# Kernel tuning notes

Hardware: AMD Instinct MI355X
Metric: run time of the kernel (lower is better)

Reference implementation:

```python
import jax, jax.numpy as jnp
import numpy as np

S, B, D, H, E, K, FF = 1024, 8, 768, 12, 8, 2, 3072


def _ln(x, w, b, eps=1e-5):
    m = x.mean(-1, keepdims=True)
    v = ((x - m) ** 2).mean(-1, keepdims=True)
    return (x - m) / jnp.sqrt(v + eps) * w + b


def setup_inputs() -> dict:
    key = jax.random.key(0)
    ks = jax.random.split(key, 12)
    s = 0.02
    return {
        "x": jax.random.normal(ks[0], (S, B, D), dtype=jnp.float32),
        "ln1_w": jnp.ones((D,), jnp.float32),
        "ln1_b": jnp.zeros((D,), jnp.float32),
        "in_proj_w": jax.random.normal(ks[1], (3 * D, D), jnp.float32) * s,
        "in_proj_b": jnp.zeros((3 * D,), jnp.float32),
        "out_proj_w": jax.random.normal(ks[2], (D, D), jnp.float32) * s,
        "out_proj_b": jnp.zeros((D,), jnp.float32),
        "ln2_w": jnp.ones((D,), jnp.float32),
        "ln2_b": jnp.zeros((D,), jnp.float32),
        "gate_w": jax.random.normal(ks[3], (E, D), jnp.float32) * s,
        "w1": jax.random.normal(ks[4], (E, D, FF), jnp.float32) * s,
        "b1": jnp.zeros((E, FF), jnp.float32),
        "w2": jax.random.normal(ks[5], (E, FF, D), jnp.float32) * s,
        "b2": jnp.zeros((E, D), jnp.float32),
    }


def reference(x, ln1_w, ln1_b, in_proj_w, in_proj_b, out_proj_w, out_proj_b,
              ln2_w, ln2_b, gate_w, w1, b1, w2, b2):
    s, b, d = x.shape
    hd = d // H
    # --- self attention (nn.MultiheadAttention, seq-first, no mask) ---
    h = _ln(x, ln1_w, ln1_b)
    qkv = h @ in_proj_w.T + in_proj_b            # [S, B, 3D]
    q, k, v = jnp.split(qkv, 3, axis=-1)

    def heads(t):
        return t.reshape(s, b, H, hd).transpose(1, 2, 0, 3)  # [B, H, S, hd]

    q, k, v = heads(q) * (hd ** -0.5), heads(k), heads(v)
    att = jax.nn.softmax(jnp.einsum('bhqd,bhkd->bhqk', q, k), axis=-1)
    o = jnp.einsum('bhqk,bhkd->bhqd', att, v).transpose(2, 0, 1, 3).reshape(s, b, d)
    o = o @ out_proj_w.T + out_proj_b
    x = x + o
    # --- MoE FFN ---
    h2 = _ln(x, ln2_w, ln2_b)
    tok = h2.reshape(-1, d)                      # [T, D], T = S*B
    logits = tok @ gate_w.T                      # [T, E]
    rw = jax.nn.softmax(logits.astype(jnp.float32), axis=-1)
    rw_top, sel = jax.lax.top_k(rw, K)           # [T, K]
    rw_top = rw_top / rw_top.sum(-1, keepdims=True)
    rw_top = rw_top.astype(tok.dtype)
    out = jnp.zeros_like(tok)
    for e in range(E):  # small fixed expert loop; math matches gather/scatter dispatch
        we = jnp.where(sel == e, rw_top, 0.0).sum(-1)       # [T] combine weight
        mid = tok @ w1[e] + b1[e]
        mid = mid * jax.nn.sigmoid(1.702 * mid)              # QuickGELU
        out = out + we[:, None] * (mid @ w2[e] + b2[e])
    return x + out.reshape(s, b, d), logits
```

## Files before the change

### kernel.cpp

```cpp
#include <hip/hip_runtime.h>
#include <stdint.h>

#define S_LEN  1024
#define BATCH  8
#define DMODEL 768
#define NHEAD  12
#define HDIM   64
#define NEXP   8
#define FFDIM  3072
#define NTOK   8192
#define D3     2304
#define NGATH  16384
#define MAXWL  136

typedef unsigned short u16;
typedef unsigned int   u32;
typedef __attribute__((ext_vector_type(8))) short bf16x8;
typedef __attribute__((ext_vector_type(4))) float f32x4;
typedef __attribute__((ext_vector_type(4))) short s16x4;

__device__ __forceinline__ u16 f2bf(float f){
  u32 x = __float_as_uint(f);
  x += 0x7fffu + ((x >> 16) & 1u);
  return (u16)(x >> 16);
}
__device__ __forceinline__ float bf2f(u16 u){
  return __uint_as_float(((u32)u) << 16);
}
__device__ __forceinline__ u32 pkbf(float a, float b){
  u32 d; asm("v_cvt_pk_bf16_f32 %0, %1, %2" : "=v"(d) : "v"(a), "v"(b)); return d;
}
__device__ __forceinline__ void gl_lds16(const void* g, void* l){
  __builtin_amdgcn_global_load_lds(
      (const __attribute__((address_space(1))) u32*)(uintptr_t)g,
      (__attribute__((address_space(3))) u32*)(u32)(uintptr_t)l,
      16, 0, 0);
}
__device__ __forceinline__ int swz64(int r){ return ((r & 7) ^ ((r >> 3) & 7)) << 4; }

__global__ __launch_bounds__(256)
void cvt_bf16(const float* __restrict__ in, u16* __restrict__ out, int n)
{
  int i = (blockIdx.x * 256 + threadIdx.x) * 4;
  if (i + 3 < n) {
    float4 v = *(const float4*)(in + i);
    out[i]     = f2bf(v.x);
    out[i + 1] = f2bf(v.y);
    out[i + 2] = f2bf(v.z);
    out[i + 3] = f2bf(v.w);
  }
}

__global__ __launch_bounds__(256)
void transpose_cvt(const float* __restrict__ in, u16* __restrict__ out, int rows, int cols)
{
  __shared__ float tile[32][33];
  const size_t eo = (size_t)blockIdx.z * rows * cols;
  in  += eo; out += eo;
  const int bx = blockIdx.x * 32, by = blockIdx.y * 32;
  const int tx = threadIdx.x, ty = threadIdx.y;
  #pragma unroll
  for (int i = 0; i < 4; i++)
    tile[ty + i * 8][tx] = in[(size_t)(by + ty + i * 8) * cols + bx + tx];
  __syncthreads();
  #pragma unroll
  for (int i = 0; i < 4; i++)
    out[(size_t)(bx + ty + i * 8) * rows + by + tx] = f2bf(tile[tx][ty + i * 8]);
}

__global__ __launch_bounds__(256)
void ln_fwd(const float* __restrict__ x, const float* __restrict__ w, const float* __restrict__ b,
            u16* __restrict__ out)
{
  const int t = blockIdx.x, tid = threadIdx.x;
  const float* xr = x + (size_t)t * DMODEL;
  const float v0 = xr[tid], v1 = xr[tid + 256], v2 = xr[tid + 512];
  float s = v0 + v1 + v2, ss = v0 * v0 + v1 * v1 + v2 * v2;
  #pragma unroll
  for (int d = 1; d < 64; d <<= 1) { s += __shfl_xor(s, d); ss += __shfl_xor(ss, d); }
  __shared__ float rs[4], rq[4];
  if ((tid & 63) == 0) { rs[tid >> 6] = s; rq[tid >> 6] = ss; }
  __syncthreads();
  s  = rs[0] + rs[1] + rs[2] + rs[3];
  ss = rq[0] + rq[1] + rq[2] + rq[3];
  const float mean = s * (1.f / DMODEL);
  const float rstd = rsqrtf(ss * (1.f / DMODEL) - mean * mean + 1e-5f);
  u16* orow = out + (size_t)t * DMODEL;
  orow[tid]       = f2bf((v0 - mean) * rstd * w[tid]       + b[tid]);
  orow[tid + 256] = f2bf((v1 - mean) * rstd * w[tid + 256] + b[tid + 256]);
  orow[tid + 512] = f2bf((v2 - mean) * rstd * w[tid + 512] + b[tid + 512]);
}

__global__ __launch_bounds__(256)
void ln2_gate(const float* __restrict__ x1, const float* __restrict__ w, const float* __restrict__ b,
              const float* __restrict__ gate_w, u16* __restrict__ h2,
              float* __restrict__ logits, float* __restrict__ selw, int* __restrict__ seli)
{
  const int t = blockIdx.x, tid = threadIdx.x;
  const float* xr = x1 + (size_t)t * DMODEL;
  const float v0 = xr[tid], v1 = xr[tid + 256], v2 = xr[tid + 512];
  float s = v0 + v1 + v2, ss = v0 * v0 + v1 * v1 + v2 * v2;
  #pragma unroll
  for (int d = 1; d < 64; d <<= 1) { s += __shfl_xor(s, d); ss += __shfl_xor(ss, d); }
  __shared__ float rs[4], rq[4];
  if ((tid & 63) == 0) { rs[tid >> 6] = s; rq[tid >> 6] = ss; }
  __syncthreads();
  s  = rs[0] + rs[1] + rs[2] + rs[3];
  ss = rq[0] + rq[1] + rq[2] + rq[3];
  const float mean = s * (1.f / DMODEL);
  const float rstd = rsqrtf(ss * (1.f / DMODEL) - mean * mean + 1e-5f);
  __shared__ float row[DMODEL];
  const float y0 = (v0 - mean) * rstd * w[tid]       + b[tid];
  const float y1 = (v1 - mean) * rstd * w[tid + 256] + b[tid + 256];
  const float y2 = (v2 - mean) * rstd * w[tid + 512] + b[tid + 512];
  row[tid] = y0; row[tid + 256] = y1; row[tid + 512] = y2;
  u16* hr = h2 + (size_t)t * DMODEL;
  hr[tid] = f2bf(y0); hr[tid + 256] = f2bf(y1); hr[tid + 512] = f2bf(y2);
  __syncthreads();
  __shared__ float lg[NEXP];
  if (tid < 64) {
    const int e = tid >> 3, j = tid & 7;
    const float* gw = gate_w + e * DMODEL;
    float a = 0.f;
    for (int d = j; d < DMODEL; d += 8) a += row[d] * gw[d];
    a += __shfl_xor(a, 1); a += __shfl_xor(a, 2); a += __shfl_xor(a, 4);
    if (j == 0) lg[e] = a;
  }
  __syncthreads();
  if (tid < NEXP) logits[(size_t)t * NEXP + tid] = lg[tid];
  if (tid == 0) {
    int ia = 0, ib = -1;
    float va = -1e30f, vb = -1e30f;
    #pragma unroll
    for (int e = 0; e < NEXP; e++) {
      const float p = lg[e];
      if (p > va)      { vb = va; ib = ia; va = p; ia = e; }
      else if (p > vb) { vb = p; ib = e; }
    }
    const float pb = __expf(vb - va);
    const float inv = 1.f / (1.f + pb);
    selw[2 * t]     = inv;
    selw[2 * t + 1] = pb * inv;
    seli[2 * t]     = ia;
    seli[2 * t + 1] = ib;
  }
}

__global__ __launch_bounds__(256)
void route_count(const int* __restrict__ seli, int* __restrict__ blkcnt)
{
  __shared__ int c[NEXP];
  const int tid = threadIdx.x;
  if (tid < NEXP) c[tid] = 0;
  __syncthreads();
  const int t = blockIdx.x * 256 + tid;
  atomicAdd(&c[seli[2 * t]], 1);
  atomicAdd(&c[seli[2 * t + 1]], 1);
  __syncthreads();
  if (tid < NEXP) blkcnt[blockIdx.x * NEXP + tid] = c[tid];
}

__global__ void route_scan(const int* __restrict__ blkcnt, int* __restrict__ offs,
                           int* __restrict__ blkbase, int* __restrict__ wl, int* __restrict__ nwork)
{
  const int tid = threadIdx.x;
  __shared__ int tot[NEXP];
  __shared__ int off_s[NEXP + 1];
  if (tid < NEXP) {
    int s = 0;
    for (int blk = 0; blk < 32; blk++) s += blkcnt[blk * NEXP + tid];
    tot[tid] = s;
  }
  __syncthreads();
  if (tid == 0) {
    int run = 0;
    for (int e = 0; e < NEXP; e++) { off_s[e] = run; run += tot[e]; }
    off_s[NEXP] = run;
    int nw = 0;
    for (int e = 0; e < NEXP; e++) {
      const int nb = (tot[e] + 127) >> 7;
      for (int i2 = 0; i2 < nb; i2++) wl[nw++] = (e << 16) | i2;
    }
    nwork[0] = nw;
  }
  __syncthreads();
  if (tid <= NEXP) offs[tid] = off_s[tid];
  if (tid < NEXP) {
    int run = off_s[tid];
    for (int blk = 0; blk < 32; blk++) { blkbase[blk * NEXP + tid] = run; run += blkcnt[blk * NEXP + tid]; }
  }
}

__global__ __launch_bounds__(256)
void route_place(const int* __restrict__ seli, const int* __restrict__ blkbase,
                 int* __restrict__ perm, int* __restrict__ posmap)
{
  __shared__ int cnts[2][4][NEXP];
  __shared__ int base[NEXP];
  const int tid = threadIdx.x, l = tid & 63, w = tid >> 6, blk = blockIdx.x;
  const int t = blk * 256 + tid;
  const unsigned long long ltm = (1ull << l) - 1ull;
  int my_e[2], my_r[2];
  my_e[0] = seli[2 * t]; my_e[1] = seli[2 * t + 1];
  my_r[0] = 0; my_r[1] = 0;
  if (tid < NEXP) base[tid] = blkbase[blk * NEXP + tid];
  #pragma unroll
  for (int k = 0; k < 2; k++) {
    #pragma unroll
    for (int ee = 0; ee < NEXP; ee++) {
      const unsigned long long msk = __ballot(my_e[k] == ee);
      if (my_e[k] == ee) my_r[k] = (int)__popcll(msk & ltm);
      if (l == ee) cnts[k][w][ee] = (int)__popcll(msk);
    }
  }
  __syncthreads();
  #pragma unroll
  for (int k = 0; k < 2; k++) {
    const int e = my_e[k];
    int pre = base[e];
    for (int k2 = 0; k2 < 2; k2++)
      for (int w2 = 0; w2 < 4; w2++)
        if (k2 < k || (k2 == k && w2 < w)) pre += cnts[k2][w2][e];
    const int pos = pre + my_r[k];
    perm[pos] = t;
    posmap[2 * t + k] = pos;
  }
}

template<int MODE>
__global__ __launch_bounds__(256)
void gemm128(const u16* __restrict__ A, const u16* __restrict__ Bw,
             int M, int N, int Kd,
             const float* __restrict__ bias, const float* __restrict__ resid,
             void* __restrict__ outp,
             const int* __restrict__ perm, const int* __restrict__ offs,
             const int* __restrict__ wl, const int* __restrict__ nwork)
{
  __shared__ u16 As[128 * 64];
  __shared__ u16 Bs[128 * 64];
  const int tid = threadIdx.x;
  const int l   = tid & 63;
  const int w   = tid >> 6;
  const int wm  = w >> 1, wn = w & 1;
  const int bn  = blockIdx.y;

  int gbase = 0, cnt = M, e = 0, bm = blockIdx.x;
  if (MODE >= 2) {
    if (blockIdx.x >= nwork[0]) return;
    const int wk = wl[blockIdx.x];
    e  = wk >> 16;
    bm = wk & 0xffff;
    gbase = offs[e];
    cnt   = offs[e + 1] - gbase;
  }
  const u16*   Bp = Bw   + (MODE >= 2 ? (size_t)e * N * Kd : 0);
  const float* bp = bias + (MODE >= 2 ? e * N : 0);

  int arow[4], acol[4], brow[4];
  #pragma unroll
  for (int i = 0; i < 4; i++) {
    const int c = tid + 256 * i;
    const int r = c >> 3;
    const int f = (r & 7) ^ ((r >> 3) & 7);
    acol[i] = ((c & 7) ^ f) * 8;
    brow[i] = bn * 128 + r;
    int g;
    if (MODE == 2)      { int gp = gbase + bm * 128 + r; if (gp > NGATH - 1) gp = NGATH - 1; g = perm[gp]; }
    else if (MODE == 3) { int gp = gbase + bm * 128 + r; if (gp > NGATH - 1) gp = NGATH - 1; g = gp; }
    else                g = bm * 128 + r;
    arow[i] = g;
  }

  f32x4 acc[4][4] = {};
  const int nk = Kd >> 6;
  for (int kt = 0; kt < nk; kt++) {
    const int kb = kt * 64;
    #pragma unroll
    for (int i = 0; i < 4; i++) {
      gl_lds16(A  + (size_t)arow[i] * Kd + kb + acol[i], &As[(i * 256 + w * 64) * 8]);
      gl_lds16(Bp + (size_t)brow[i] * Kd + kb + acol[i], &Bs[(i * 256 + w * 64) * 8]);
    }
    __syncthreads();
    #pragma unroll
    for (int ks = 0; ks < 2; ks++) {
      bf16x8 af[4], bv[4];
      #pragma unroll
      for (int m = 0; m < 4; m++) {
        const int row = wm * 64 + m * 16 + (l & 15);
        af[m] = *(const bf16x8*)((const char*)As +
                  ((row * 128 + ks * 64 + (l >> 4) * 16) ^ swz64(row)));
      }
      #pragma unroll
      for (int n = 0; n < 4; n++) {
        const int row = wn * 64 + n * 16 + (l & 15);
        bv[n] = *(const bf16x8*)((const char*)Bs +
                  ((row * 128 + ks * 64 + (l >> 4) * 16) ^ swz64(row)));
      }
      #pragma unroll
      for (int m = 0; m < 4; m++)
        #pragma unroll
        for (int n = 0; n < 4; n++)
          acc[m][n] = __builtin_amdgcn_mfma_f32_16x16x32_bf16(bv[n], af[m], acc[m][n], 0, 0, 0);
    }
    __syncthreads();
  }

  f32x4 biasv[4];
  int   c0[4];
  #pragma unroll
  for (int n = 0; n < 4; n++) {
    c0[n] = bn * 128 + wn * 64 + n * 16 + ((l >> 4) << 2);
    biasv[n] = *(const f32x4*)(bp + c0[n]);
  }
  #pragma unroll
  for (int m = 0; m < 4; m++) {
    const int row = bm * 128 + wm * 64 + m * 16 + (l & 15);
    #pragma unroll
    for (int n = 0; n < 4; n++) {
      f32x4 v = acc[m][n] + biasv[n];
      if (MODE == 0) {
        *(uint2*)((u16*)outp + (size_t)row * N + c0[n]) =
            make_uint2(pkbf(v[0], v[1]), pkbf(v[2], v[3]));
      } else if (MODE == 1) {
        const size_t o = (size_t)row * N + c0[n];
        f32x4 rv = *(const f32x4*)(resid + o);
        v += rv;
        *(f32x4*)((float*)outp + o) = v;
      } else if (MODE == 2) {
        if (row < cnt) {
          #pragma unroll
          for (int r = 0; r < 4; r++)
            v[r] = v[r] * __builtin_amdgcn_rcpf(1.f + __expf(-1.702f * v[r]));
          *(uint2*)((u16*)outp + (size_t)(gbase + row) * FFDIM + c0[n]) =
              make_uint2(pkbf(v[0], v[1]), pkbf(v[2], v[3]));
        }
      } else {
        if (row < cnt)
          *(uint2*)((u16*)outp + (size_t)(gbase + row) * DMODEL + c0[n]) =
              make_uint2(pkbf(v[0], v[1]), pkbf(v[2], v[3]));
      }
    }
  }
}

__global__ __launch_bounds__(256)
void attn_fwd(const u16* __restrict__ qkv, u16* __restrict__ o)
{
  __shared__ u16 Ksw[64 * 64];
  __shared__ u16 Vt [64 * 64];
  __shared__ u16 Pl [4 * 16 * 64];
  const int tid = threadIdx.x;
  const int l   = tid & 63, w = tid >> 6;
  const int qt  = blockIdx.x;
  const int b_  = blockIdx.y / NHEAD;
  const int hh  = blockIdx.y % NHEAD;

  const int qrow = qt * 64 + w * 16 + (l & 15);
  const size_t qoff = ((size_t)(qrow * BATCH + b_)) * D3 + hh * HDIM + (l >> 4) * 8;
  const bf16x8 qa0 = *(const bf16x8*)&qkv[qoff];
  const bf16x8 qa1 = *(const bf16x8*)&qkv[qoff + 32];

  f32x4 oacc[4] = {};
  float m_[4], l_[4];
  #pragma unroll
  for (int r = 0; r < 4; r++) { m_[r] = -1e30f; l_[r] = 0.f; }

  u16* Pw = Pl + w * 1024;
  const int pswz = swz64(l & 15);

  for (int kt = 0; kt < 16; kt++) {
    #pragma unroll
    for (int i = 0; i < 2; i++) {
      const int c = tid + 256 * i;
      const int key = c >> 3, dimb = (c & 7) * 8;
      const size_t gb = ((size_t)((kt * 64 + key) * BATCH + b_)) * D3 + hh * HDIM + dimb;
      const bf16x8 kd = *(const bf16x8*)&qkv[gb + DMODEL];
      const bf16x8 vd = *(const bf16x8*)&qkv[gb + 2 * DMODEL];
      *(bf16x8*)((char*)Ksw + ((key * 128 + dimb * 2) ^ swz64(key))) = kd;
      #pragma unroll
      for (int j = 0; j < 8; j++) {
        const int dim = dimb + j;
        *(u16*)((char*)Vt + ((dim * 128 + key * 2) ^ swz64(dim))) = (u16)vd[j];
      }
    }
    __syncthreads();

    f32x4 sc[4] = {};
    #pragma unroll
    for (int kb2 = 0; kb2 < 4; kb2++) {
      const int key = kb2 * 16 + (l & 15);
      const int ksz = swz64(key);
      #pragma unroll
      for (int ks = 0; ks < 2; ks++) {
        const bf16x8 kf = *(const bf16x8*)((char*)Ksw +
            ((key * 128 + (ks * 32 + (l >> 4) * 8) * 2) ^ ksz));
        sc[kb2] = __builtin_amdgcn_mfma_f32_16x16x32_bf16(ks ? qa1 : qa0, kf, sc[kb2], 0, 0, 0);
      }
    }
    #pragma unroll
    for (int kb2 = 0; kb2 < 4; kb2++)
      #pragma unroll
      for (int r = 0; r < 4; r++) sc[kb2][r] *= 0.125f;

    float nm[4], corr[4], ps[4];
    #pragma unroll
    for (int r = 0; r < 4; r++) {
      float pm = fmaxf(fmaxf(sc[0][r], sc[1][r]), fmaxf(sc[2][r], sc[3][r]));
      pm = fmaxf(pm, __shfl_xor(pm, 1));
      pm = fmaxf(pm, __shfl_xor(pm, 2));
      pm = fmaxf(pm, __shfl_xor(pm, 4));
      pm = fmaxf(pm, __shfl_xor(pm, 8));
      nm[r]   = fmaxf(m_[r], pm);
      corr[r] = __expf(m_[r] - nm[r]);
      m_[r]   = nm[r];
      ps[r]   = 0.f;
    }
    #pragma unroll
    for (int kb2 = 0; kb2 < 4; kb2++) {
      #pragma unroll
      for (int r = 0; r < 4; r++) {
        const float p = __expf(sc[kb2][r] - nm[r]);
        ps[r] += p;
        const int prow = (l >> 4) * 4 + r;
        const int pcol = kb2 * 16 + (l & 15);
        *(u16*)((char*)Pw + ((prow * 128 + pcol * 2) ^ swz64(prow))) = f2bf(p);
      }
    }
    #pragma unroll
    for (int r = 0; r < 4; r++) {
      float s = ps[r];
      s += __shfl_xor(s, 1); s += __shfl_xor(s, 2);
      s += __shfl_xor(s, 4); s += __shfl_xor(s, 8);
      l_[r] = l_[r] * corr[r] + s;
      #pragma unroll
      for (int ob = 0; ob < 4; ob++) oacc[ob][r] *= corr[r];
    }

    #pragma unroll
    for (int ob = 0; ob < 4; ob++) {
      const int dim = ob * 16 + (l & 15);
      const int vsz = swz64(dim);
      #pragma unroll
      for (int ks = 0; ks < 2; ks++) {
        const int kko = (ks * 32 + (l >> 4) * 8) * 2;
        const bf16x8 pf = *(const bf16x8*)((char*)Pw + (((l & 15) * 128 + kko) ^ pswz));
        const bf16x8 vf = *(const bf16x8*)((char*)Vt + ((dim * 128 + kko) ^ vsz));
        oacc[ob] = __builtin_amdgcn_mfma_f32_16x16x32_bf16(pf, vf, oacc[ob], 0, 0, 0);
      }
    }
    __syncthreads();
  }

  #pragma unroll
  for (int r = 0; r < 4; r++) {
    const float inv = 1.f / l_[r];
    const int qs = qt * 64 + w * 16 + (l >> 4) * 4 + r;
    #pragma unroll
    for (int ob = 0; ob < 4; ob++)
      o[((size_t)(qs * BATCH + b_)) * DMODEL + hh * HDIM + ob * 16 + (l & 15)] =
          f2bf(oacc[ob][r] * inv);
  }
}

__global__ __launch_bounds__(192)
void moe_combine(const float* __restrict__ x1, const u16* __restrict__ eout,
                 const int* __restrict__ posmap, const float* __restrict__ selw,
                 float* __restrict__ out)
{
  const int t = blockIdx.x, j = threadIdx.x;
  const int p0 = posmap[2 * t], p1 = posmap[2 * t + 1];
  const float w0 = selw[2 * t], w1 = selw[2 * t + 1];
  const float4 xv = ((const float4*)(x1 + (size_t)t * DMODEL))[j];
  const s16x4 a = ((const s16x4*)(eout + (size_t)p0 * DMODEL))[j];
  const s16x4 c = ((const s16x4*)(eout + (size_t)p1 * DMODEL))[j];
  float4 r;
  r.x = xv.x + w0 * bf2f((u16)a[0]) + w1 * bf2f((u16)c[0]);
  r.y = xv.y + w0 * bf2f((u16)a[1]) + w1 * bf2f((u16)c[1]);
  r.z = xv.z + w0 * bf2f((u16)a[2]) + w1 * bf2f((u16)c[2]);
  r.w = xv.w + w0 * bf2f((u16)a[3]) + w1 * bf2f((u16)c[3]);
  ((float4*)(out + (size_t)t * DMODEL))[j] = r;
}

#define MB (1ull << 20)
static const size_t OFF_H    = 0;
static const size_t OFF_QKV  = 16 * MB;
static const size_t OFF_O    = 54 * MB;
static const size_t OFF_IPW  = 67 * MB;
static const size_t OFF_OPW  = 71 * MB;
static const size_t OFF_MID  = 0;
static const size_t OFF_X1   = 101 * MB;
static const size_t OFF_H2   = 127 * MB;
static const size_t OFF_W1T  = 140 * MB;
static const size_t OFF_W2T  = 178 * MB;
static const size_t OFF_EOUT = 216 * MB;
static const size_t OFF_SELW = 242 * MB;
static const size_t OFF_PERM = 242 * MB + (1 << 16);
static const size_t OFF_POS  = 242 * MB + (2 << 16);
static const size_t OFF_SELI = 242 * MB + (3 << 16);
static const size_t OFF_BCNT = 242 * MB + (4 << 16);
static const size_t OFF_BBASE= 242 * MB + (4 << 16) + 4096;
static const size_t OFF_OFFS = 242 * MB + (4 << 16) + 8192;
static const size_t OFF_WL   = 242 * MB + (5 << 16);
static const size_t OFF_NW   = 242 * MB + (5 << 16) + 1024;

extern "C" void kernel_launch(void* const* d_in, const int* in_sizes, int n_in,
                              void* d_out, int out_size, void* d_ws, size_t ws_size,
                              hipStream_t stream)
{
  const float* x     = (const float*)d_in[0];
  const float* ln1w  = (const float*)d_in[1];
  const float* ln1b  = (const float*)d_in[2];
  const float* ipw_f = (const float*)d_in[3];
  const float* ipb   = (const float*)d_in[4];
  const float* opw_f = (const float*)d_in[5];
  const float* opb   = (const float*)d_in[6];
  const float* ln2w  = (const float*)d_in[7];
  const float* ln2b  = (const float*)d_in[8];
  const float* gatew = (const float*)d_in[9];
  const float* w1    = (const float*)d_in[10];
  const float* b1    = (const float*)d_in[11];
  const float* w2    = (const float*)d_in[12];
  const float* b2    = (const float*)d_in[13];

  char* ws = (char*)d_ws;
  u16*   h    = (u16*)(ws + OFF_H);
  u16*   qkv  = (u16*)(ws + OFF_QKV);
  u16*   ob   = (u16*)(ws + OFF_O);
  u16*   ipw  = (u16*)(ws + OFF_IPW);
  u16*   opw  = (u16*)(ws + OFF_OPW);
  u16*   mid  = (u16*)(ws + OFF_MID);
  float* x1   = (float*)(ws + OFF_X1);
  u16*   h2   = (u16*)(ws + OFF_H2);
  u16*   w1t  = (u16*)(ws + OFF_W1T);
  u16*   w2t  = (u16*)(ws + OFF_W2T);
  u16*   eout = (u16*)(ws + OFF_EOUT);
  float* selw = (float*)(ws + OFF_SELW);
  int*   perm = (int*)(ws + OFF_PERM);
  int*   posm = (int*)(ws + OFF_POS);
  int*   seli = (int*)(ws + OFF_SELI);
  int*   bcnt = (int*)(ws + OFF_BCNT);
  int*   bbas = (int*)(ws + OFF_BBASE);
  int*   offs = (int*)(ws + OFF_OFFS);
  int*   wl   = (int*)(ws + OFF_WL);
  int*   nwork= (int*)(ws + OFF_NW);
  float* outx  = (float*)d_out;
  float* outlg = outx + (size_t)NTOK * DMODEL;

  cvt_bf16<<<(D3 * DMODEL) / 1024, 256, 0, stream>>>(ipw_f, ipw, D3 * DMODEL);
  cvt_bf16<<<(DMODEL * DMODEL) / 1024, 256, 0, stream>>>(opw_f, opw, DMODEL * DMODEL);
  transpose_cvt<<<dim3(FFDIM / 32, DMODEL / 32, NEXP), dim3(32, 8), 0, stream>>>(w1, w1t, DMODEL, FFDIM);
  transpose_cvt<<<dim3(DMODEL / 32, FFDIM / 32, NEXP), dim3(32, 8), 0, stream>>>(w2, w2t, FFDIM, DMODEL);

  ln_fwd<<<NTOK, 256, 0, stream>>>(x, ln1w, ln1b, h);
  gemm128<0><<<dim3(NTOK / 128, D3 / 128, 1), 256, 0, stream>>>(
      h, ipw, NTOK, D3, DMODEL, ipb, nullptr, qkv, nullptr, nullptr, nullptr, nullptr);
  attn_fwd<<<dim3(S_LEN / 64, BATCH * NHEAD), 256, 0, stream>>>(qkv, ob);
  gemm128<1><<<dim3(NTOK / 128, DMODEL / 128, 1), 256, 0, stream>>>(
      ob, opw, NTOK, DMODEL, DMODEL, opb, x, x1, nullptr, nullptr, nullptr, nullptr);

  ln2_gate<<<NTOK, 256, 0, stream>>>(x1, ln2w, ln2b, gatew, h2, outlg, selw, seli);
  route_count<<<32, 256, 0, stream>>>(seli, bcnt);
  route_scan<<<1, 64, 0, stream>>>(bcnt, offs, bbas, wl, nwork);
  route_place<<<32, 256, 0, stream>>>(seli, bbas, perm, posm);

  gemm128<2><<<dim3(MAXWL, FFDIM / 128, 1), 256, 0, stream>>>(
      h2, w1t, NGATH, FFDIM, DMODEL, b1, nullptr, mid, perm, offs, wl, nwork);
  gemm128<3><<<dim3(MAXWL, DMODEL / 128, 1), 256, 0, stream>>>(
      mid, w2t, NGATH, DMODEL, FFDIM, b2, nullptr, eout, nullptr, offs, wl, nwork);

  moe_combine<<<NTOK, 192, 0, stream>>>(x1, eout, posm, selw, outx);
}
```

Before: 561.9 us.

## Double-buffer LDS tiles in gemm128 to overlap global loads with MFMA

```diff
diff --git a/kernel.cpp b/kernel.cpp
--- a/kernel.cpp
+++ b/kernel.cpp
@@ -236,8 +236,8 @@
              const int* __restrict__ perm, const int* __restrict__ offs,
              const int* __restrict__ wl, const int* __restrict__ nwork)
 {
-  __shared__ u16 As[128 * 64];
-  __shared__ u16 Bs[128 * 64];
+  __shared__ u16 As[2][128 * 64];
+  __shared__ u16 Bs[2][128 * 64];
   const int tid = threadIdx.x;
   const int l   = tid & 63;
   const int w   = tid >> 6;
@@ -273,27 +273,43 @@
 
   f32x4 acc[4][4] = {};
   const int nk = Kd >> 6;
+
+  #pragma unroll
+  for (int i = 0; i < 4; i++) {
+    gl_lds16(A  + (size_t)arow[i] * Kd + acol[i], &As[0][(i * 256 + w * 64) * 8]);
+    gl_lds16(Bp + (size_t)brow[i] * Kd + acol[i], &Bs[0][(i * 256 + w * 64) * 8]);
+  }
+
+  int cur = 0;
   for (int kt = 0; kt < nk; kt++) {
-    const int kb = kt * 64;
-    #pragma unroll
-    for (int i = 0; i < 4; i++) {
-      gl_lds16(A  + (size_t)arow[i] * Kd + kb + acol[i], &As[(i * 256 + w * 64) * 8]);
-      gl_lds16(Bp + (size_t)brow[i] * Kd + kb + acol[i], &Bs[(i * 256 + w * 64) * 8]);
-    }
-    __syncthreads();
+    const bool pf = (kt + 1 < nk);
+    if (pf) {
+      const int kb = (kt + 1) * 64;
+      #pragma unroll
+      for (int i = 0; i < 4; i++) {
+        gl_lds16(A  + (size_t)arow[i] * Kd + kb + acol[i], &As[cur ^ 1][(i * 256 + w * 64) * 8]);
+        gl_lds16(Bp + (size_t)brow[i] * Kd + kb + acol[i], &Bs[cur ^ 1][(i * 256 + w * 64) * 8]);
+      }
+      asm volatile("s_waitcnt vmcnt(8)" ::: "memory");
+    } else {
+      asm volatile("s_waitcnt vmcnt(0)" ::: "memory");
+    }
+    __builtin_amdgcn_s_barrier();
+    __builtin_amdgcn_sched_barrier(0);
+
     #pragma unroll
     for (int ks = 0; ks < 2; ks++) {
       bf16x8 af[4], bv[4];
       #pragma unroll
       for (int m = 0; m < 4; m++) {
         const int row = wm * 64 + m * 16 + (l & 15);
-        af[m] = *(const bf16x8*)((const char*)As +
+        af[m] = *(const bf16x8*)((const char*)&As[cur][0] +
                   ((row * 128 + ks * 64 + (l >> 4) * 16) ^ swz64(row)));
       }
       #pragma unroll
       for (int n = 0; n < 4; n++) {
         const int row = wn * 64 + n * 16 + (l & 15);
-        bv[n] = *(const bf16x8*)((const char*)Bs +
+        bv[n] = *(const bf16x8*)((const char*)&Bs[cur][0] +
                   ((row * 128 + ks * 64 + (l >> 4) * 16) ^ swz64(row)));
       }
       #pragma unroll
@@ -302,7 +318,8 @@
         for (int n = 0; n < 4; n++)
           acc[m][n] = __builtin_amdgcn_mfma_f32_16x16x32_bf16(bv[n], af[m], acc[m][n], 0, 0, 0);
     }
-    __syncthreads();
+    if (pf) __builtin_amdgcn_s_barrier();
+    cur ^= 1;
   }
 
   f32x4 biasv[4];
```

Result: faster. 546.7 us, median of 2 (-2.7%).
